# Kernel optimization log

Measured on AMD Instinct MI355X. Metric: run time of the kernel, lower is better.

Reference implementation:

```python
import jax, jax.numpy as jnp
import numpy as np

B, T, C, H = 8, 1024, 1024, 16
D = C // H
EPS = 1e-5


def setup_inputs() -> dict:
    key = jax.random.key(0)
    ks = jax.random.split(key, 12)
    s = lambda k, shape, scale=0.02: jax.random.normal(k, shape, dtype=jnp.float32) * scale
    return {
        "x": jax.random.normal(ks[0], (B, T, C), dtype=jnp.float32),
        "ln1_w": jnp.ones((C,), jnp.float32),
        "ln1_b": jnp.zeros((C,), jnp.float32),
        "w_qkv": s(ks[1], (C, 3 * C)),
        "b_qkv": jnp.zeros((3 * C,), jnp.float32),
        "w_o": s(ks[2], (C, C)),
        "b_o": jnp.zeros((C,), jnp.float32),
        "ln2_w": jnp.ones((C,), jnp.float32),
        "ln2_b": jnp.zeros((C,), jnp.float32),
        "w_fc": s(ks[3], (C, 4 * C)),
        "b_fc": jnp.zeros((4 * C,), jnp.float32),
        "w_proj": s(ks[4], (4 * C, C)),
        "b_proj": jnp.zeros((C,), jnp.float32),
    }


def _layernorm(x, w, b):
    mu = jnp.mean(x, axis=-1, keepdims=True)
    var = jnp.mean(jnp.square(x - mu), axis=-1, keepdims=True)
    return (x - mu) * jax.lax.rsqrt(var + EPS) * w + b


def _attention(x, w_qkv, b_qkv, w_o, b_o):
    b, t, c = x.shape
    qkv = x @ w_qkv + b_qkv                      # [B,T,3C]
    q, k, v = jnp.split(qkv, 3, axis=-1)
    q = q.reshape(b, t, H, D)
    k = k.reshape(b, t, H, D)
    v = v.reshape(b, t, H, D)
    scores = jnp.einsum("bqhd,bkhd->bhqk", q, k) / jnp.sqrt(jnp.float32(D))
    mask = jnp.tril(jnp.ones((t, t), dtype=bool))  # causal
    scores = jnp.where(mask, scores, jnp.float32(-jnp.inf))
    att = jax.nn.softmax(scores, axis=-1)
    y = jnp.einsum("bhqk,bkhd->bqhd", att, v).reshape(b, t, c)
    return y @ w_o + b_o


def _mlp(x, w_fc, b_fc, w_proj, b_proj):
    h = jax.nn.gelu(x @ w_fc + b_fc, approximate=True)  # tanh GELU
    return h @ w_proj + b_proj


def reference(x, ln1_w, ln1_b, w_qkv, b_qkv, w_o, b_o, ln2_w, ln2_b, w_fc, b_fc, w_proj, b_proj):
    x = x + _attention(_layernorm(x, ln1_w, ln1_b), w_qkv, b_qkv, w_o, b_o)
    x = x + _mlp(_layernorm(x, ln2_w, ln2_b), w_fc, b_fc, w_proj, b_proj)
    return x
```

## Files before the change

kernel.cpp:

```cpp
#include <hip/hip_runtime.h>
#include <math.h>
#include <stdint.h>

typedef unsigned short u16;
typedef unsigned int u32;
typedef __attribute__((ext_vector_type(4))) unsigned short u16x4;
typedef __attribute__((ext_vector_type(8))) unsigned short u16x8;
typedef __attribute__((ext_vector_type(8))) __bf16 bf16x8;
typedef __attribute__((ext_vector_type(4))) float f32x4;

#define Bn 8
#define Tn 1024
#define Cn 1024
#define Hn 16
#define Dn 64
#define Mn 8192

#define F32_ONE_BITS 0x3F800000u

__device__ __forceinline__ float b2f(u16 u) {
  union { unsigned int i; float f; } v; v.i = ((unsigned int)u) << 16; return v.f;
}
__device__ __forceinline__ u16 f2b(float f) {
  union { float f; unsigned int i; } v; v.f = f;
  unsigned int r = v.i + 0x7fffu + ((v.i >> 16) & 1u);
  return (u16)(r >> 16);
}

__device__ __forceinline__ void async_ld16(const u16* g, u16* l) {
  __builtin_amdgcn_global_load_lds(
      (__attribute__((address_space(1))) void*)g,
      (__attribute__((address_space(3))) void*)l, 16, 0, 0);
}

template <int N> __device__ __forceinline__ void wait_vmcnt() {
  if constexpr (N == 8)      asm volatile("s_waitcnt vmcnt(8)" ::: "memory");
  else if constexpr (N == 6) asm volatile("s_waitcnt vmcnt(6)" ::: "memory");
  else                       asm volatile("s_waitcnt vmcnt(0)" ::: "memory");
}
__device__ __forceinline__ void raw_barrier() {
  asm volatile("s_barrier" ::: "memory");
}

__device__ __forceinline__ float gelu_fast(float x) {
  float u2 = 1.5957691216057308f * (x + 0.044715f * x * x * x);
  return x / (1.0f + __expf(-u2));
}

__global__ __launch_bounds__(256) void cvt_x_k(const void* __restrict__ src, u16* __restrict__ dst,
                                               const u32* __restrict__ flagp) {
  bool isf32 = (*flagp == F32_ONE_BITS);
  size_t i = ((size_t)blockIdx.x * 256 + threadIdx.x) * 4;
  if (isf32) {
    f32x4 v = *reinterpret_cast<const f32x4*>((const float*)src + i);
    u16x4 o;
#pragma unroll
    for (int j = 0; j < 4; j++) o[j] = f2b(v[j]);
    *reinterpret_cast<u16x4*>(dst + i) = o;
  } else {
    *reinterpret_cast<u16x4*>(dst + i) = *reinterpret_cast<const u16x4*>((const u16*)src + i);
  }
}

struct SmallCvt { const void* src[8]; u16* dst[8]; int n[8]; };

__global__ __launch_bounds__(256) void cvt_small_k(SmallCvt p, const u32* __restrict__ flagp) {
  bool isf32 = (*flagp == F32_ONE_BITS);
  int t = blockIdx.x * 256 + threadIdx.x;
  int off = 0;
#pragma unroll
  for (int i = 0; i < 8; i++) {
    int idx = t - off;
    if (idx >= 0 && idx < p.n[i]) {
      u16 v = isf32 ? f2b(((const float*)p.src[i])[idx]) : ((const u16*)p.src[i])[idx];
      p.dst[i][idx] = v;
    }
    off += p.n[i];
  }
}

__global__ __launch_bounds__(256) void transpose_k(const void* __restrict__ in,
                                                   u16* __restrict__ out, int K, int N,
                                                   const u32* __restrict__ flagp) {
  bool isf32 = (*flagp == F32_ONE_BITS);
  __shared__ u16 tile[32][33];
  int c0 = blockIdx.x * 32, r0 = blockIdx.y * 32;
  int tx = threadIdx.x, ty = threadIdx.y;
#pragma unroll
  for (int i = 0; i < 4; i++) {
    size_t idx = (size_t)(r0 + ty + i * 8) * N + c0 + tx;
    tile[ty + i * 8][tx] = isf32 ? f2b(((const float*)in)[idx]) : ((const u16*)in)[idx];
  }
  __syncthreads();
#pragma unroll
  for (int i = 0; i < 4; i++)
    out[(size_t)(c0 + ty + i * 8) * K + r0 + tx] = tile[tx][ty + i * 8];
}

__global__ __launch_bounds__(256) void ln_k(const u16* __restrict__ x, const u16* __restrict__ w,
                                            const u16* __restrict__ bi, u16* __restrict__ out) {
  int row = blockIdx.x, tid = threadIdx.x;
  const u16* xr = x + (size_t)row * Cn;
  u16x4 xv = *reinterpret_cast<const u16x4*>(xr + tid * 4);
  float v0 = b2f(xv[0]), v1 = b2f(xv[1]), v2 = b2f(xv[2]), v3 = b2f(xv[3]);
  float s = v0 + v1 + v2 + v3;
  float s2 = v0 * v0 + v1 * v1 + v2 * v2 + v3 * v3;
#pragma unroll
  for (int m = 1; m < 64; m <<= 1) {
    s += __shfl_xor(s, m, 64);
    s2 += __shfl_xor(s2, m, 64);
  }
  __shared__ float rs_[4], rs2_[4];
  int wave = tid >> 6, lane = tid & 63;
  if (lane == 0) { rs_[wave] = s; rs2_[wave] = s2; }
  __syncthreads();
  s = rs_[0] + rs_[1] + rs_[2] + rs_[3];
  s2 = rs2_[0] + rs2_[1] + rs2_[2] + rs2_[3];
  float mu = s * (1.0f / Cn);
  float var = s2 * (1.0f / Cn) - mu * mu;
  float rstd = rsqrtf(var + 1e-5f);
  u16x4 wv = *reinterpret_cast<const u16x4*>(w + tid * 4);
  u16x4 bv = *reinterpret_cast<const u16x4*>(bi + tid * 4);
  u16x4 ov;
  float vv[4] = {v0, v1, v2, v3};
#pragma unroll
  for (int j = 0; j < 4; j++)
    ov[j] = f2b((vv[j] - mu) * rstd * b2f(wv[j]) + b2f(bv[j]));
  *reinterpret_cast<u16x4*>(out + (size_t)row * Cn + tid * 4) = ov;
}

template <int BN_T, int GELU, int RES, int F32OUT>
__global__ __launch_bounds__(512, 2) void gemm2_k(const u16* __restrict__ A, const u16* __restrict__ BT,
                                                  const u16* __restrict__ bias, const u16* __restrict__ res,
                                                  void* __restrict__ Cout, int M, int N, int K) {
  constexpr int NI = BN_T / 64;
  constexpr int NB = NI;
  constexpr int L = 4 + NB;

  __shared__ __align__(16) u16 As[2 * 256 * 64];
  __shared__ __align__(16) u16 Bs[2 * BN_T * 64];

  int tid = threadIdx.x, wave = tid >> 6, lane = tid & 63;
  int l15 = lane & 15, quad = lane >> 4;

  int nbx = gridDim.x;
  int nwg = nbx * gridDim.y;
  int lin = blockIdx.y * nbx + blockIdx.x;
  int cpx = nwg >> 3;
  int swz = (lin & 7) * cpx + (lin >> 3);
  int m0 = (swz / nbx) * 256;
  int n0 = (swz % nbx) * BN_T;

  int wm = (wave >> 2) * 128;
  int wn = (wave & 3) * (NI * 16);

  int offAb[2], offBb[2];
#pragma unroll
  for (int kc = 0; kc < 2; kc++) {
    int x = ((kc * 4 + quad) ^ (l15 & 7)) * 8;
    offAb[kc] = (wm + l15) * 64 + x;
    offBb[kc] = (wn + l15) * 64 + x;
  }

  const u16* aS[4]; int aD[4];
#pragma unroll
  for (int i = 0; i < 4; i++) {
    int c = i * 512 + tid;
    int row = c >> 3, j = (c & 7) ^ (row & 7);
    aS[i] = A + (size_t)(m0 + row) * K + j * 8;
    aD[i] = c * 8;
  }
  const u16* bS[NB]; int bD[NB];
#pragma unroll
  for (int i = 0; i < NB; i++) {
    int c = i * 512 + tid;
    int row = c >> 3, j = (c & 7) ^ (row & 7);
    bS[i] = BT + (size_t)(n0 + row) * K + j * 8;
    bD[i] = c * 8;
  }

#define STAGE(KT, BSEL)                                                      \
  do {                                                                       \
    u16* ab_ = As + (BSEL) * (256 * 64);                                     \
    u16* bb_ = Bs + (BSEL) * (BN_T * 64);                                    \
    _Pragma("unroll")                                                        \
    for (int i_ = 0; i_ < 4; i_++)                                           \
      async_ld16(aS[i_] + (size_t)(KT) * 64, ab_ + aD[i_]);                  \
    _Pragma("unroll")                                                        \
    for (int i_ = 0; i_ < NB; i_++)                                          \
      async_ld16(bS[i_] + (size_t)(KT) * 64, bb_ + bD[i_]);                  \
  } while (0)

  f32x4 acc[8][NI];
#pragma unroll
  for (int mi = 0; mi < 8; mi++)
#pragma unroll
    for (int ni = 0; ni < NI; ni++) acc[mi][ni] = (f32x4){0.f, 0.f, 0.f, 0.f};

  int NT = K >> 6;

  STAGE(0, 0);
  STAGE(1, 1);
  wait_vmcnt<L>();
  raw_barrier();

  for (int t = 0; t < NT; ++t) {
    const u16* Ab = As + (t & 1) * (256 * 64);
    const u16* Bb = Bs + (t & 1) * (BN_T * 64);

    __builtin_amdgcn_s_setprio(1);
    bf16x8 bv[NI][2];
#pragma unroll
    for (int ni = 0; ni < NI; ni++)
#pragma unroll
      for (int kc = 0; kc < 2; kc++)
        bv[ni][kc] = *reinterpret_cast<const bf16x8*>(Bb + offBb[kc] + ni * 1024);
#pragma unroll
    for (int mi = 0; mi < 8; mi++) {
      bf16x8 av0 = *reinterpret_cast<const bf16x8*>(Ab + offAb[0] + mi * 1024);
      bf16x8 av1 = *reinterpret_cast<const bf16x8*>(Ab + offAb[1] + mi * 1024);
#pragma unroll
      for (int ni = 0; ni < NI; ni++) {
        acc[mi][ni] = __builtin_amdgcn_mfma_f32_16x16x32_bf16(av0, bv[ni][0], acc[mi][ni], 0, 0, 0);
        acc[mi][ni] = __builtin_amdgcn_mfma_f32_16x16x32_bf16(av1, bv[ni][1], acc[mi][ni], 0, 0, 0);
      }
    }
    __builtin_amdgcn_s_setprio(0);

    raw_barrier();
    if (t + 2 < NT) {
      STAGE(t + 2, (t & 1));
      wait_vmcnt<L>();
    } else {
      wait_vmcnt<0>();
    }
    raw_barrier();
  }
#undef STAGE

#pragma unroll
  for (int ni = 0; ni < NI; ni++) {
    int col = n0 + wn + ni * 16 + l15;
    float bval = b2f(bias[col]);
#pragma unroll
    for (int mi = 0; mi < 8; mi++) {
#pragma unroll
      for (int r = 0; r < 4; r++) {
        int row = m0 + wm + mi * 16 + quad * 4 + r;
        float v = acc[mi][ni][r] + bval;
        if (GELU) v = gelu_fast(v);
        if (RES) v += b2f(res[(size_t)row * N + col]);
        if (F32OUT)
          ((float*)Cout)[(size_t)row * N + col] = v;
        else
          ((u16*)Cout)[(size_t)row * N + col] = f2b(v);
      }
    }
  }
}

#define ATTN_PROC(QF, O, M_R, L_R, Q0, KV0, KSB)                                      \
  do {                                                                                \
    float sv[4][4];                                                                   \
    _Pragma("unroll")                                                                 \
    for (int ni = 0; ni < 4; ni++) {                                                  \
      f32x4 z = (f32x4){0.f, 0.f, 0.f, 0.f};                                          \
      _Pragma("unroll")                                                               \
      for (int kc = 0; kc < 2; kc++) {                                                \
        bf16x8 bfr = *reinterpret_cast<const bf16x8*>((KSB) + offKb[kc] + ni * 1024); \
        z = __builtin_amdgcn_mfma_f32_16x16x32_bf16(QF[kc], bfr, z, 0, 0, 0);         \
      }                                                                               \
      _Pragma("unroll")                                                               \
      for (int r = 0; r < 4; r++) sv[ni][r] = z[r];                                   \
    }                                                                                 \
    bool diag = ((KV0) + 64 > (Q0));                                                  \
    _Pragma("unroll")                                                                 \
    for (int ni = 0; ni < 4; ni++)                                                    \
      _Pragma("unroll")                                                               \
      for (int r = 0; r < 4; r++) {                                                   \
        float v = sv[ni][r] * 0.125f;                                                 \
        if (diag && ((KV0) + ni * 16 + l15 > (Q0) + quad * 4 + r)) v = -1e30f;        \
        sv[ni][r] = v;                                                                \
      }                                                                               \
    float mt[4], al[4], rs[4];                                                        \
    _Pragma("unroll")                                                                 \
    for (int r = 0; r < 4; r++) {                                                     \
      mt[r] = fmaxf(fmaxf(sv[0][r], sv[1][r]), fmaxf(sv[2][r], sv[3][r]));            \
      _Pragma("unroll")                                                               \
      for (int m = 1; m <= 8; m <<= 1) mt[r] = fmaxf(mt[r], __shfl_xor(mt[r], m, 64));\
      float mn = fmaxf(M_R[r], mt[r]);                                                \
      al[r] = __expf(M_R[r] - mn);                                                    \
      M_R[r] = mn;                                                                    \
      rs[r] = 0.f;                                                                    \
    }                                                                                 \
    _Pragma("unroll")                                                                 \
    for (int ni = 0; ni < 4; ni++)                                                    \
      _Pragma("unroll")                                                               \
      for (int r = 0; r < 4; r++) {                                                   \
        float p = __expf(sv[ni][r] - M_R[r]);                                         \
        sv[ni][r] = p;                                                                \
        rs[r] += p;                                                                   \
      }                                                                               \
    _Pragma("unroll")                                                                 \
    for (int r = 0; r < 4; r++) {                                                     \
      _Pragma("unroll")                                                               \
      for (int m = 1; m <= 8; m <<= 1) rs[r] += __shfl_xor(rs[r], m, 64);             \
      L_R[r] = L_R[r] * al[r] + rs[r];                                                \
    }                                                                                 \
    _Pragma("unroll")                                                                 \
    for (int dn = 0; dn < 4; dn++)                                                    \
      _Pragma("unroll")                                                               \
      for (int r = 0; r < 4; r++) O[dn][r] *= al[r];                                  \
    _Pragma("unroll")                                                                 \
    for (int ni = 0; ni < 4; ni++)                                                    \
      _Pragma("unroll")                                                               \
      for (int r = 0; r < 4; r++)                                                     \
        Ps[wave][pwBase + r * 72 + ni * 16] = f2b(sv[ni][r]);                         \
    _Pragma("unroll")                                                                 \
    for (int kc = 0; kc < 2; kc++) {                                                  \
      bf16x8 afr = *reinterpret_cast<const bf16x8*>(&Ps[wave][prBase + kc * 32]);     \
      _Pragma("unroll")                                                               \
      for (int dn = 0; dn < 4; dn++) {                                                \
        bf16x8 bfr = *reinterpret_cast<const bf16x8*>(&VTs[vrBase + dn * 1152 + kc * 32]); \
        O[dn] = __builtin_amdgcn_mfma_f32_16x16x32_bf16(afr, bfr, O[dn], 0, 0, 0);    \
      }                                                                               \
    }                                                                                 \
  } while (0)

__global__ __launch_bounds__(256, 4) void attn_k(const u16* __restrict__ qkv, u16* __restrict__ y) {
  int bh = blockIdx.x;
  int lo = blockIdx.y;
  int hi = 15 - lo;
  int b = bh >> 4, h = bh & 15;
  int tid = threadIdx.x, wave = tid >> 6, lane = tid & 63;
  int l15 = lane & 15, quad = lane >> 4;

  __shared__ __align__(16) u16 Ks[2][64 * 64];
  __shared__ __align__(16) u16 VTs[64 * 72];
  __shared__ __align__(16) u16 Ps[4][16 * 72];

  const u16* base = qkv + (size_t)b * Tn * 3072 + h * 64;
  int q0_lo = lo * 64 + wave * 16;
  int q0_hi = hi * 64 + wave * 16;

  bf16x8 qf_lo[2], qf_hi[2];
#pragma unroll
  for (int kc = 0; kc < 2; kc++) {
    qf_lo[kc] = *reinterpret_cast<const bf16x8*>(base + (size_t)(q0_lo + l15) * 3072 + kc * 32 + quad * 8);
    qf_hi[kc] = *reinterpret_cast<const bf16x8*>(base + (size_t)(q0_hi + l15) * 3072 + kc * 32 + quad * 8);
  }

  int offKb[2];
#pragma unroll
  for (int kc = 0; kc < 2; kc++)
    offKb[kc] = l15 * 64 + (((kc * 4 + quad) ^ (l15 & 7)) * 8);

  int kSrcOff[2], kDstOff[2];
#pragma unroll
  for (int i = 0; i < 2; i++) {
    int c = wave * 128 + i * 64 + lane;
    int row = c >> 3, j = (c & 7) ^ (row & 7);
    kSrcOff[i] = row * 3072 + j * 8;
    kDstOff[i] = c * 8;
  }
  const u16* kBase = base + 1024;
  const u16* vBase = base + 2048;
  int kp = tid & 31, dgroup = tid >> 5;
  u32* vtw = reinterpret_cast<u32*>(VTs);

#pragma unroll
  for (int i = 0; i < 2; i++) async_ld16(kBase + kSrcOff[i], &Ks[0][kDstOff[i]]);
  u16x8 va, vb;
  {
    const u16* vS = vBase + (size_t)(2 * kp) * 3072 + dgroup * 8;
    va = *reinterpret_cast<const u16x8*>(vS);
    vb = *reinterpret_cast<const u16x8*>(vS + 3072);
  }

  f32x4 o_lo[4], o_hi[4];
  float m_lo[4], l_lo[4], m_hi[4], l_hi[4];
#pragma unroll
  for (int i = 0; i < 4; i++) {
    o_lo[i] = (f32x4){0.f, 0.f, 0.f, 0.f};
    o_hi[i] = (f32x4){0.f, 0.f, 0.f, 0.f};
    m_lo[i] = -1e30f; m_hi[i] = -1e30f;
    l_lo[i] = 0.f;    l_hi[i] = 0.f;
  }

  int pwBase = quad * 4 * 72 + l15;
  int prBase = l15 * 72 + quad * 8;
  int vrBase = l15 * 72 + quad * 8;

  int kvend_hi = hi * 64, kvend_lo = lo * 64;
  int buf = 0;
  for (int kv0 = 0; kv0 <= kvend_hi; kv0 += 64) {
    __syncthreads();
#pragma unroll
    for (int i = 0; i < 8; i++)
      vtw[(dgroup * 8 + i) * 36 + kp] = (u32)va[i] | ((u32)vb[i] << 16);
    __syncthreads();
    if (kv0 + 64 <= kvend_hi) {
      const u16* kS = kBase + (size_t)(kv0 + 64) * 3072;
#pragma unroll
      for (int i = 0; i < 2; i++) async_ld16(kS + kSrcOff[i], &Ks[buf ^ 1][kDstOff[i]]);
      const u16* vS = vBase + (size_t)(kv0 + 64 + 2 * kp) * 3072 + dgroup * 8;
      va = *reinterpret_cast<const u16x8*>(vS);
      vb = *reinterpret_cast<const u16x8*>(vS + 3072);
    }
    {
      const u16* KsB = &Ks[buf][0];
      ATTN_PROC(qf_hi, o_hi, m_hi, l_hi, q0_hi, kv0, KsB);
      if (kv0 <= kvend_lo)
        ATTN_PROC(qf_lo, o_lo, m_lo, l_lo, q0_lo, kv0, KsB);
    }
    buf ^= 1;
  }

#pragma unroll
  for (int r = 0; r < 4; r++) {
    float inv = 1.0f / l_hi[r];
    int row = b * Tn + q0_hi + quad * 4 + r;
#pragma unroll
    for (int dn = 0; dn < 4; dn++)
      y[(size_t)row * Cn + h * 64 + dn * 16 + l15] = f2b(o_hi[dn][r] * inv);
  }
#pragma unroll
  for (int r = 0; r < 4; r++) {
    float inv = 1.0f / l_lo[r];
    int row = b * Tn + q0_lo + quad * 4 + r;
#pragma unroll
    for (int dn = 0; dn < 4; dn++)
      y[(size_t)row * Cn + h * 64 + dn * 16 + l15] = f2b(o_lo[dn][r] * inv);
  }
}

extern "C" void kernel_launch(void* const* d_in, const int* in_sizes, int n_in,
                              void* d_out, int out_size, void* d_ws, size_t ws_size,
                              hipStream_t stream) {
  const void* x      = d_in[0];
  const void* ln1_w  = d_in[1];
  const void* ln1_b  = d_in[2];
  const void* w_qkv  = d_in[3];
  const void* b_qkv  = d_in[4];
  const void* w_o    = d_in[5];
  const void* b_o    = d_in[6];
  const void* ln2_w  = d_in[7];
  const void* ln2_b  = d_in[8];
  const void* w_fc   = d_in[9];
  const void* b_fc   = d_in[10];
  const void* w_proj = d_in[11];
  const void* b_proj = d_in[12];
  const u32* flagp = (const u32*)ln1_w;

  size_t off = 0;
  char* wsb = (char*)d_ws;
  auto alloc = [&](size_t bytes) {
    void* p = wsb + off;
    off += (bytes + 255) & ~(size_t)255;
    return (u16*)p;
  };
  u16* wqkvT  = alloc((size_t)3072 * 1024 * 2);
  u16* woT    = alloc((size_t)1024 * 1024 * 2);
  u16* wfcT   = alloc((size_t)4096 * 1024 * 2);
  u16* wprojT = alloc((size_t)1024 * 4096 * 2);
  u16* xb     = alloc((size_t)Mn * 1024 * 2);
  u16* sm     = alloc((size_t)16384 * 2);
  u16* xn     = alloc((size_t)Mn * 1024 * 2);
  u16* ybuf   = alloc((size_t)Mn * 1024 * 2);
  u16* x1     = alloc((size_t)Mn * 1024 * 2);
  u16* big    = alloc((size_t)Mn * 4096 * 2);
  u16* qkvbuf = big;
  u16* hbuf   = big;
  if (off > ws_size) return;

  u16* LW1 = sm;
  u16* LB1 = sm + 1024;
  u16* BQKV = sm + 2048;
  u16* BO  = sm + 5120;
  u16* LW2 = sm + 6144;
  u16* LB2 = sm + 7168;
  u16* BFC = sm + 8192;
  u16* BPJ = sm + 12288;

  SmallCvt sc;
  sc.src[0] = ln1_w;  sc.dst[0] = LW1;  sc.n[0] = 1024;
  sc.src[1] = ln1_b;  sc.dst[1] = LB1;  sc.n[1] = 1024;
  sc.src[2] = b_qkv;  sc.dst[2] = BQKV; sc.n[2] = 3072;
  sc.src[3] = b_o;    sc.dst[3] = BO;   sc.n[3] = 1024;
  sc.src[4] = ln2_w;  sc.dst[4] = LW2;  sc.n[4] = 1024;
  sc.src[5] = ln2_b;  sc.dst[5] = LB2;  sc.n[5] = 1024;
  sc.src[6] = b_fc;   sc.dst[6] = BFC;  sc.n[6] = 4096;
  sc.src[7] = b_proj; sc.dst[7] = BPJ;  sc.n[7] = 1024;

  hipLaunchKernelGGL(cvt_small_k, dim3(52), dim3(256), 0, stream, sc, flagp);
  hipLaunchKernelGGL(cvt_x_k, dim3(Mn * 1024 / 4 / 256), dim3(256), 0, stream, x, xb, flagp);

  dim3 tb(32, 8);
  hipLaunchKernelGGL(transpose_k, dim3(3072 / 32, 1024 / 32), tb, 0, stream, w_qkv, wqkvT, 1024, 3072, flagp);
  hipLaunchKernelGGL(transpose_k, dim3(1024 / 32, 1024 / 32), tb, 0, stream, w_o, woT, 1024, 1024, flagp);
  hipLaunchKernelGGL(transpose_k, dim3(4096 / 32, 1024 / 32), tb, 0, stream, w_fc, wfcT, 1024, 4096, flagp);
  hipLaunchKernelGGL(transpose_k, dim3(1024 / 32, 4096 / 32), tb, 0, stream, w_proj, wprojT, 4096, 1024, flagp);

  hipLaunchKernelGGL(ln_k, dim3(Mn), dim3(256), 0, stream, xb, LW1, LB1, xn);
  hipLaunchKernelGGL((gemm2_k<256, 0, 0, 0>), dim3(3072 / 256, Mn / 256), dim3(512), 0, stream,
                     xn, wqkvT, BQKV, (const u16*)nullptr, (void*)qkvbuf, Mn, 3072, 1024);
  hipLaunchKernelGGL(attn_k, dim3(Bn * Hn, 8), dim3(256), 0, stream, qkvbuf, ybuf);
  hipLaunchKernelGGL((gemm2_k<128, 0, 1, 0>), dim3(1024 / 128, Mn / 256), dim3(512), 0, stream,
                     ybuf, woT, BO, xb, (void*)x1, Mn, 1024, 1024);
  hipLaunchKernelGGL(ln_k, dim3(Mn), dim3(256), 0, stream, x1, LW2, LB2, xn);
  hipLaunchKernelGGL((gemm2_k<256, 1, 0, 0>), dim3(4096 / 256, Mn / 256), dim3(512), 0, stream,
                     xn, wfcT, BFC, (const u16*)nullptr, (void*)hbuf, Mn, 4096, 1024);
  hipLaunchKernelGGL((gemm2_k<128, 0, 1, 1>), dim3(1024 / 128, Mn / 256), dim3(512), 0, stream,
                     hbuf, wprojT, BPJ, x1, d_out, Mn, 1024, 4096);
}
```

Before: 532.1 us.

## Split GEMM k-loop into four phases interleaving async loads with MFMAs

The bf16 GEMM main loop is split into four sub-phases over A row-halves and k-halves. Global-to-LDS async loads are spread across those phases instead of being issued in one burst after compute. Loads for the next tile's A chunks 1 and 3 are delayed one iteration, and chunks of tile t+2 are written into the current buffer once their rows have been consumed. The goal is to overlap memory traffic with MFMA work and shorten the idle gap at the end of each iteration. In exchange there are four barriers per iteration instead of two, and the vmcnt bookkeeping is more intricate.

```diff
diff --git a/kernel.cpp b/kernel.cpp
--- a/kernel.cpp
+++ b/kernel.cpp
@@ -36,6 +36,7 @@
 template <int N> __device__ __forceinline__ void wait_vmcnt() {
   if constexpr (N == 8)      asm volatile("s_waitcnt vmcnt(8)" ::: "memory");
   else if constexpr (N == 6) asm volatile("s_waitcnt vmcnt(6)" ::: "memory");
+  else if constexpr (N == 4) asm volatile("s_waitcnt vmcnt(4)" ::: "memory");
   else                       asm volatile("s_waitcnt vmcnt(0)" ::: "memory");
 }
 __device__ __forceinline__ void raw_barrier() {
@@ -130,15 +131,16 @@
 }
 
 template <int BN_T, int GELU, int RES, int F32OUT>
-__global__ __launch_bounds__(512, 2) void gemm2_k(const u16* __restrict__ A, const u16* __restrict__ BT,
+__global__ __launch_bounds__(512, 2) void gemm3_k(const u16* __restrict__ A, const u16* __restrict__ BT,
                                                   const u16* __restrict__ bias, const u16* __restrict__ res,
                                                   void* __restrict__ Cout, int M, int N, int K) {
   constexpr int NI = BN_T / 64;
   constexpr int NB = NI;
-  constexpr int L = 4 + NB;
-
-  __shared__ __align__(16) u16 As[2 * 256 * 64];
-  __shared__ __align__(16) u16 Bs[2 * BN_T * 64];
+  constexpr int AE = 256 * 64;
+  constexpr int BE = BN_T * 64;
+
+  __shared__ __align__(16) u16 As[2 * AE];
+  __shared__ __align__(16) u16 Bs[2 * BE];
 
   int tid = threadIdx.x, wave = tid >> 6, lane = tid & 63;
   int l15 = lane & 15, quad = lane >> 4;
@@ -154,12 +156,14 @@
   int wm = (wave >> 2) * 128;
   int wn = (wave & 3) * (NI * 16);
 
-  int offAb[2], offBb[2];
-#pragma unroll
-  for (int kc = 0; kc < 2; kc++) {
-    int x = ((kc * 4 + quad) ^ (l15 & 7)) * 8;
-    offAb[kc] = (wm + l15) * 64 + x;
-    offBb[kc] = (wn + l15) * 64 + x;
+  int offA0, offA1, offB0, offB1;
+  {
+    int x0 = ((0 + quad) ^ (l15 & 7)) * 8;
+    int x1 = ((4 + quad) ^ (l15 & 7)) * 8;
+    offA0 = (wm + l15) * 64 + x0;
+    offA1 = (wm + l15) * 64 + x1;
+    offB0 = (wn + l15) * 64 + x0;
+    offB1 = (wn + l15) * 64 + x1;
   }
 
   const u16* aS[4]; int aD[4];
@@ -179,17 +183,10 @@
     bD[i] = c * 8;
   }
 
-#define STAGE(KT, BSEL)                                                      \
-  do {                                                                       \
-    u16* ab_ = As + (BSEL) * (256 * 64);                                     \
-    u16* bb_ = Bs + (BSEL) * (BN_T * 64);                                    \
-    _Pragma("unroll")                                                        \
-    for (int i_ = 0; i_ < 4; i_++)                                           \
-      async_ld16(aS[i_] + (size_t)(KT) * 64, ab_ + aD[i_]);                  \
-    _Pragma("unroll")                                                        \
-    for (int i_ = 0; i_ < NB; i_++)                                          \
-      async_ld16(bS[i_] + (size_t)(KT) * 64, bb_ + bD[i_]);                  \
-  } while (0)
+#define ISSA(T, I) async_ld16(aS[I] + (size_t)(T) * 64, &As[((T) & 1) * AE + aD[I]])
+#define ISSB(T, I) async_ld16(bS[I] + (size_t)(T) * 64, &Bs[((T) & 1) * BE + bD[I]])
+#define LDF(P) (*reinterpret_cast<const bf16x8*>(P))
+#define MM(AV, BV, CC) CC = __builtin_amdgcn_mfma_f32_16x16x32_bf16(AV, BV, CC, 0, 0, 0)
 
   f32x4 acc[8][NI];
 #pragma unroll
@@ -199,44 +196,117 @@
 
   int NT = K >> 6;
 
-  STAGE(0, 0);
-  STAGE(1, 1);
-  wait_vmcnt<L>();
+#pragma unroll
+  for (int i = 0; i < 4; i++) ISSA(0, i);
+#pragma unroll
+  for (int i = 0; i < NB; i++) ISSB(0, i);
+#pragma unroll
+  for (int i = 0; i < 4; i++) ISSA(1, i);
+#pragma unroll
+  for (int i = 0; i < NB; i++) ISSB(1, i);
+  wait_vmcnt<4 + NB>();
   raw_barrier();
 
+  bf16x8 bv[NI][2];
+
+#pragma unroll 2
   for (int t = 0; t < NT; ++t) {
-    const u16* Ab = As + (t & 1) * (256 * 64);
-    const u16* Bb = Bs + (t & 1) * (BN_T * 64);
-
-    __builtin_amdgcn_s_setprio(1);
-    bf16x8 bv[NI][2];
-#pragma unroll
-    for (int ni = 0; ni < NI; ni++)
-#pragma unroll
-      for (int kc = 0; kc < 2; kc++)
-        bv[ni][kc] = *reinterpret_cast<const bf16x8*>(Bb + offBb[kc] + ni * 1024);
-#pragma unroll
-    for (int mi = 0; mi < 8; mi++) {
-      bf16x8 av0 = *reinterpret_cast<const bf16x8*>(Ab + offAb[0] + mi * 1024);
-      bf16x8 av1 = *reinterpret_cast<const bf16x8*>(Ab + offAb[1] + mi * 1024);
+    const u16* Ab = &As[(t & 1) * AE];
+    const u16* Bb = &Bs[(t & 1) * BE];
+    bool haveN = (t >= 1) && (t + 1 < NT);
+    bool haveNN = (t + 2 < NT);
+
+    {
+      bf16x8 a0 = LDF(Ab + offA0);
+      bf16x8 a1 = LDF(Ab + offA0 + 1024);
+      bf16x8 a2 = LDF(Ab + offA0 + 2048);
+      bf16x8 a3 = LDF(Ab + offA0 + 3072);
+#pragma unroll
+      for (int ni = 0; ni < NI; ni++) bv[ni][0] = LDF(Bb + offB0 + ni * 1024);
+      if (haveN) ISSA(t + 1, 1);
+      raw_barrier();
+      __builtin_amdgcn_s_setprio(1);
 #pragma unroll
       for (int ni = 0; ni < NI; ni++) {
-        acc[mi][ni] = __builtin_amdgcn_mfma_f32_16x16x32_bf16(av0, bv[ni][0], acc[mi][ni], 0, 0, 0);
-        acc[mi][ni] = __builtin_amdgcn_mfma_f32_16x16x32_bf16(av1, bv[ni][1], acc[mi][ni], 0, 0, 0);
-      }
-    }
-    __builtin_amdgcn_s_setprio(0);
-
-    raw_barrier();
-    if (t + 2 < NT) {
-      STAGE(t + 2, (t & 1));
-      wait_vmcnt<L>();
-    } else {
-      wait_vmcnt<0>();
-    }
-    raw_barrier();
-  }
-#undef STAGE
+        MM(a0, bv[ni][0], acc[0][ni]);
+        MM(a1, bv[ni][0], acc[1][ni]);
+        MM(a2, bv[ni][0], acc[2][ni]);
+        MM(a3, bv[ni][0], acc[3][ni]);
+      }
+      __builtin_amdgcn_s_setprio(0);
+      raw_barrier();
+    }
+    {
+      bf16x8 a0 = LDF(Ab + offA1);
+      bf16x8 a1 = LDF(Ab + offA1 + 1024);
+      bf16x8 a2 = LDF(Ab + offA1 + 2048);
+      bf16x8 a3 = LDF(Ab + offA1 + 3072);
+#pragma unroll
+      for (int ni = 0; ni < NI; ni++) bv[ni][1] = LDF(Bb + offB1 + ni * 1024);
+      if (haveN) ISSA(t + 1, 3);
+      raw_barrier();
+      __builtin_amdgcn_s_setprio(1);
+#pragma unroll
+      for (int ni = 0; ni < NI; ni++) {
+        MM(a0, bv[ni][1], acc[0][ni]);
+        MM(a1, bv[ni][1], acc[1][ni]);
+        MM(a2, bv[ni][1], acc[2][ni]);
+        MM(a3, bv[ni][1], acc[3][ni]);
+      }
+      __builtin_amdgcn_s_setprio(0);
+      raw_barrier();
+    }
+    {
+      bf16x8 a0 = LDF(Ab + offA0 + 4096);
+      bf16x8 a1 = LDF(Ab + offA0 + 5120);
+      bf16x8 a2 = LDF(Ab + offA0 + 6144);
+      bf16x8 a3 = LDF(Ab + offA0 + 7168);
+      if (haveNN) {
+        ISSA(t + 2, 0);
+        ISSB(t + 2, 0);
+        if constexpr (NB == 4) ISSB(t + 2, 1);
+      }
+      raw_barrier();
+      __builtin_amdgcn_s_setprio(1);
+#pragma unroll
+      for (int ni = 0; ni < NI; ni++) {
+        MM(a0, bv[ni][0], acc[4][ni]);
+        MM(a1, bv[ni][0], acc[5][ni]);
+        MM(a2, bv[ni][0], acc[6][ni]);
+        MM(a3, bv[ni][0], acc[7][ni]);
+      }
+      __builtin_amdgcn_s_setprio(0);
+      raw_barrier();
+    }
+    {
+      bf16x8 a0 = LDF(Ab + offA1 + 4096);
+      bf16x8 a1 = LDF(Ab + offA1 + 5120);
+      bf16x8 a2 = LDF(Ab + offA1 + 6144);
+      bf16x8 a3 = LDF(Ab + offA1 + 7168);
+      if (haveNN) {
+        ISSA(t + 2, 2);
+        if constexpr (NB == 4) { ISSB(t + 2, 2); ISSB(t + 2, 3); }
+        else ISSB(t + 2, 1);
+      }
+      raw_barrier();
+      __builtin_amdgcn_s_setprio(1);
+#pragma unroll
+      for (int ni = 0; ni < NI; ni++) {
+        MM(a0, bv[ni][1], acc[4][ni]);
+        MM(a1, bv[ni][1], acc[5][ni]);
+        MM(a2, bv[ni][1], acc[6][ni]);
+        MM(a3, bv[ni][1], acc[7][ni]);
+      }
+      __builtin_amdgcn_s_setprio(0);
+      if (haveNN) wait_vmcnt<2 + NB>();
+      else wait_vmcnt<0>();
+      raw_barrier();
+    }
+  }
+#undef ISSA
+#undef ISSB
+#undef LDF
+#undef MM
 
 #pragma unroll
   for (int ni = 0; ni < NI; ni++) {
@@ -502,14 +572,14 @@
   hipLaunchKernelGGL(transpose_k, dim3(1024 / 32, 4096 / 32), tb, 0, stream, w_proj, wprojT, 4096, 1024, flagp);
 
   hipLaunchKernelGGL(ln_k, dim3(Mn), dim3(256), 0, stream, xb, LW1, LB1, xn);
-  hipLaunchKernelGGL((gemm2_k<256, 0, 0, 0>), dim3(3072 / 256, Mn / 256), dim3(512), 0, stream,
+  hipLaunchKernelGGL((gemm3_k<256, 0, 0, 0>), dim3(3072 / 256, Mn / 256), dim3(512), 0, stream,
                      xn, wqkvT, BQKV, (const u16*)nullptr, (void*)qkvbuf, Mn, 3072, 1024);
   hipLaunchKernelGGL(attn_k, dim3(Bn * Hn, 8), dim3(256), 0, stream, qkvbuf, ybuf);
-  hipLaunchKernelGGL((gemm2_k<128, 0, 1, 0>), dim3(1024 / 128, Mn / 256), dim3(512), 0, stream,
+  hipLaunchKernelGGL((gemm3_k<128, 0, 1, 0>), dim3(1024 / 128, Mn / 256), dim3(512), 0, stream,
                      ybuf, woT, BO, xb, (void*)x1, Mn, 1024, 1024);
   hipLaunchKernelGGL(ln_k, dim3(Mn), dim3(256), 0, stream, x1, LW2, LB2, xn);
-  hipLaunchKernelGGL((gemm2_k<256, 1, 0, 0>), dim3(4096 / 256, Mn / 256), dim3(512), 0, stream,
+  hipLaunchKernelGGL((gemm3_k<256, 1, 0, 0>), dim3(4096 / 256, Mn / 256), dim3(512), 0, stream,
                      xn, wfcT, BFC, (const u16*)nullptr, (void*)hbuf, Mn, 4096, 1024);
-  hipLaunchKernelGGL((gemm2_k<128, 0, 1, 1>), dim3(1024 / 128, Mn / 256), dim3(512), 0, stream,
+  hipLaunchKernelGGL((gemm3_k<128, 0, 1, 1>), dim3(1024 / 128, Mn / 256), dim3(512), 0, stream,
                      hbuf, wprojT, BPJ, x1, d_out, Mn, 1024, 4096);
 }
```

Result: slower. 547.5 us (+2.9%).
